# Performance work log

Measured on AMD Instinct MI355X. Metric: run time of the kernel, lower is better.

Reference implementation:

```python
import math
import jax, jax.numpy as jnp
import numpy as np

LOW_FREQ = 1
FACTOR = 1


def setup_inputs() -> dict:
    key = jax.random.key(0)
    x = jax.random.normal(key, (16, 4096, 256), dtype=jnp.float32)
    return {"x": x}


def reference(x):
    b, t, d = x.shape
    x_freq = jnp.fft.rfft(x, axis=1)  # (b, t//2+1, d) complex
    if t % 2 == 0:
        x_freq = x_freq[:, LOW_FREQ:-1]
        f = jnp.fft.rfftfreq(t)[LOW_FREQ:-1]
    else:
        x_freq = x_freq[:, LOW_FREQ:]
        f = jnp.fft.rfftfreq(t)[LOW_FREQ:]
    f = f.astype(jnp.float32)
    F = x_freq.shape[1]
    top_k = int(FACTOR * math.log(F))  # static (shape-derived)

    # top-k by magnitude along freq axis, independently per (b, d)
    xf_bdf = jnp.moveaxis(x_freq, 1, 2)              # (b, d, F)
    _, idx = jax.lax.top_k(jnp.abs(xf_bdf), top_k)   # (b, d, k) int32
    xf_sel = jnp.take_along_axis(xf_bdf, idx, axis=2)  # (b, d, k)
    xf_sel = jnp.moveaxis(xf_sel, 2, 1)              # (b, k, d)
    f_sel = jnp.moveaxis(f[idx], 2, 1)[:, :, None, :]  # (b, k, 1, d)

    # extrapolate: conj-pair frequencies, synthesize cosines, reduce over freq
    xf2 = jnp.concatenate([xf_sel, jnp.conj(xf_sel)], axis=1)  # (b, 2k, d)
    f2 = jnp.concatenate([f_sel, -f_sel], axis=1)              # (b, 2k, 1, d)
    tt = jnp.arange(t, dtype=jnp.float32)[None, None, :, None]  # (1,1,t,1)
    amp = (jnp.abs(xf2) * 2.0 / t)[:, :, None, :]   # (b, 2k, 1, d)
    phase = jnp.angle(xf2)[:, :, None, :]           # (b, 2k, 1, d)
    x_time = amp * jnp.cos(2.0 * math.pi * f2 * tt + phase)  # (b, 2k, t, d)
    return x_time.sum(axis=1)  # (b, t, d)
```

## Files before the change

### kernel.cpp

```cpp
#include <hip/hip_runtime.h>
#include <math.h>

#define T_LEN 4096
#define N2    2048
#define TOPK  7
#define NCH   256
#define R8F 0.70710678f

#define AD(a) ((a) + ((a) >> 3) + ((a) >> 8))

typedef float nt_f4 __attribute__((ext_vector_type(4)));

typedef float2 c32;
__device__ __forceinline__ c32 cadd(c32 a, c32 b) { return make_float2(a.x + b.x, a.y + b.y); }
__device__ __forceinline__ c32 csub(c32 a, c32 b) { return make_float2(a.x - b.x, a.y - b.y); }
__device__ __forceinline__ c32 cmul(c32 a, c32 w) {
    return make_float2(w.x * a.x - w.y * a.y, w.x * a.y + w.y * a.x);
}
__device__ __forceinline__ c32 csq(c32 a) {
    return make_float2(a.x * a.x - a.y * a.y, 2.0f * a.x * a.y);
}
__device__ __forceinline__ c32 mulnegi(c32 a) { return make_float2(a.y, -a.x); }

__device__ __forceinline__ void dft8_pw(c32 x[8], c32 w1)
{
    c32 t0 = cadd(x[0], x[4]), t4 = csub(x[0], x[4]);
    c32 t1 = cadd(x[1], x[5]), t5 = csub(x[1], x[5]);
    c32 t2 = cadd(x[2], x[6]), t6 = csub(x[2], x[6]);
    c32 t3 = cadd(x[3], x[7]), t7 = csub(x[3], x[7]);
    c32 s0 = cadd(t0, t2), s2 = csub(t0, t2);
    c32 s1 = cadd(t1, t3), s3 = csub(t1, t3);
    x[0] = cadd(s0, s1);
    x[4] = csub(s0, s1);
    c32 s3n = mulnegi(s3);
    x[2] = cadd(s2, s3n);
    x[6] = csub(s2, s3n);
    c32 c1 = make_float2(R8F * (t5.x + t5.y), R8F * (t5.y - t5.x));
    c32 c2 = mulnegi(t6);
    c32 c3 = make_float2(R8F * (t7.y - t7.x), -R8F * (t7.x + t7.y));
    c32 d0 = cadd(t4, c2), d1 = csub(t4, c2);
    c32 d2 = cadd(c1, c3), d3 = csub(c1, c3);
    x[1] = cadd(d0, d2);
    x[5] = csub(d0, d2);
    c32 d3n = mulnegi(d3);
    x[3] = cadd(d1, d3n);
    x[7] = csub(d1, d3n);

    c32 w2 = csq(w1);
    c32 w3 = cmul(w1, w2);
    c32 w4 = csq(w2);
    c32 w5 = cmul(w3, w2);
    c32 w6 = csq(w3);
    c32 w7 = cmul(w4, w3);
    x[1] = cmul(x[1], w1);
    x[2] = cmul(x[2], w2);
    x[3] = cmul(x[3], w3);
    x[4] = cmul(x[4], w4);
    x[5] = cmul(x[5], w5);
    x[6] = cmul(x[6], w6);
    x[7] = cmul(x[7], w7);
}

__global__ __launch_bounds__(256) void prep_kernel(
    const float* __restrict__ x, float2* __restrict__ gz,
    double2* __restrict__ tw, float2* __restrict__ twf)
{
    if (blockIdx.x < 16) {
        int p = blockIdx.x * 256 + threadIdx.x;
        double th = -2.0 * 3.14159265358979323846 * (double)p / (double)T_LEN;
        double c = cos(th), s = sin(th);
        tw[p]  = make_double2(c, s);
        twf[p] = make_float2((float)c, (float)s);
        return;
    }
    __shared__ float tile[256][32];
    const int bid = blockIdx.x - 16;
    const int jt = bid & 15;
    const int ct = (bid >> 4) & 7;
    const int b  = bid >> 7;
    const int j0 = jt << 4, c0 = ct << 5;
    const int tid = threadIdx.x;

    const float* src = x + (size_t)b * T_LEN * NCH + c0;
#pragma unroll
    for (int s = 0; s < 8; ++s) {
        int fid = tid + (s << 8);
        int lr  = fid >> 3;
        int qc  = (fid & 7) << 2;
        int t   = (j0 << 1) + ((lr >> 5) << 9) + (lr & 31);
        nt_f4 v = __builtin_nontemporal_load(
            (const nt_f4*)(src + (size_t)t * NCH + qc));
        int sc = qc ^ ((((lr & 7) ^ ((lr >> 3) & 7))) << 2);
        *(nt_f4*)&tile[lr][sc] = v;
    }
    __syncthreads();

    const int dj = tid & 15;
    const int j  = j0 + dj;
    float ang = (float)j * -0.00306796157577128218f;
    float s1v, c1v;
    __sincosf(ang, &s1v, &c1v);
    c32 w1 = make_float2(c1v, s1v);

    for (int h = 0; h < 2; ++h) {
        const int cc = (tid >> 4) + (h << 4);
        c32 xx[8];
#pragma unroll
        for (int u = 0; u < 8; ++u) {
            int lr0 = (u << 5) + (dj << 1);
            int lr1 = lr0 + 1;
            int s0  = cc ^ ((((lr0 & 7) ^ ((lr0 >> 3) & 7))) << 2);
            int s1  = cc ^ ((((lr1 & 7) ^ ((lr1 >> 3) & 7))) << 2);
            xx[u] = make_float2(tile[lr0][s0], tile[lr1][s1]);
        }
        dft8_pw(xx, w1);
        float2* gcol = gz + ((size_t)((b << 8) + c0 + cc)) * N2;
#pragma unroll
        for (int m = 0; m < 8; ++m)
            gcol[(m << 8) + j] = xx[m];
    }
}

__device__ __forceinline__ unsigned long long packkey32(float mag, int k) {
    return ((unsigned long long)__float_as_uint(mag) << 32)
         | (unsigned long long)(2047 - k);
}

#define CSWAP(i, j) { unsigned long long a_ = keys[i], b_ = keys[j]; \
                      keys[i] = a_ > b_ ? a_ : b_; keys[j] = a_ > b_ ? b_ : a_; }

__global__ __launch_bounds__(256, 8) void fft_topk_kernel(
    const float* __restrict__ xt, const double2* __restrict__ tw,
    const float2* __restrict__ twf,
    int* __restrict__ k_out, float4* __restrict__ ab4)
{
    __shared__ float2 zz[AD(N2 - 1) + 3];
    __shared__ unsigned long long wavetop[4 * TOPK];
    __shared__ unsigned long long selkey[TOPK];

    const int tid = threadIdx.x;
    const int bc  = blockIdx.x;
    const float2* gcol = ((const float2*)xt) + (size_t)bc * N2;

    c32 x[8];
    {
        const int g = tid >> 5, j2 = tid & 31, base = (g << 8) + j2;
#pragma unroll
        for (int u = 0; u < 8; ++u)
            x[u] = gcol[base + (u << 5)];
        dft8_pw(x, twf[16 * j2]);
#pragma unroll
        for (int m = 0; m < 8; ++m)
            zz[AD(base + (m << 5))] = x[m];
    }
    __syncthreads();

    {
        const int g3 = tid >> 2, j3 = tid & 3, base = (g3 << 5) + j3;
#pragma unroll
        for (int u = 0; u < 8; ++u)
            x[u] = zz[AD(base + (u << 2))];
        dft8_pw(x, twf[128 * j3]);
#pragma unroll
        for (int m = 0; m < 8; ++m)
            zz[AD(base + (m << 2))] = x[m];
    }
    __syncthreads();

#pragma unroll
    for (int q = 0; q < 2; ++q) {
        int h4 = ((q << 8) + tid) << 2;
#pragma unroll
        for (int r = 0; r < 4; ++r)
            x[q * 4 + r] = zz[AD(h4 + r)];
    }
    __syncthreads();
#pragma unroll
    for (int q = 0; q < 2; ++q) {
        c32 b0 = x[q*4+0], b1 = x[q*4+1], b2 = x[q*4+2], b3 = x[q*4+3];
        c32 e0 = cadd(b0, b2), e1 = csub(b0, b2);
        c32 e2 = cadd(b1, b3), e3 = csub(b1, b3);
        c32 e3n = mulnegi(e3);
        int kbase = ((tid & 7) << 6) | (((tid >> 3) & 7) << 3) | (q << 2) | (tid >> 6);
        zz[AD(kbase)]        = cadd(e0, e2);
        zz[AD(kbase + 1024)] = csub(e0, e2);
        zz[AD(kbase +  512)] = cadd(e1, e3n);
        zz[AD(kbase + 1536)] = csub(e1, e3n);
    }
    __syncthreads();

    unsigned long long keys[8];
#pragma unroll
    for (int j = 0; j < 4; ++j) {
        int k  = 1 + tid + (j << 8);
        int kp = N2 - k;
        float2 yk = zz[AD(k)];
        float2 yp = zz[AD(kp)];
        float Ar = 0.5f * (yk.x + yp.x), Ai = 0.5f * (yk.y - yp.y);
        float Br = 0.5f * (yk.y + yp.y), Bi = -0.5f * (yk.x - yp.x);
        float2 t = twf[k];
        float Cr = t.x * Br - t.y * Bi;
        float Ci = t.x * Bi + t.y * Br;
        float m1 = (Ar + Cr) * (Ar + Cr) + (Ai + Ci) * (Ai + Ci);
        float m2 = (Ar - Cr) * (Ar - Cr) + (Ai - Ci) * (Ai - Ci);
        keys[2 * j]     = packkey32(m1, k);
        keys[2 * j + 1] = (kp != k) ? packkey32(m2, kp) : 0ULL;
    }

    CSWAP(0,1) CSWAP(2,3) CSWAP(4,5) CSWAP(6,7)
    CSWAP(0,2) CSWAP(1,3) CSWAP(4,6) CSWAP(5,7)
    CSWAP(1,2) CSWAP(5,6)
    CSWAP(0,4) CSWAP(1,5) CSWAP(2,6) CSWAP(3,7)
    CSWAP(2,4) CSWAP(3,5)
    CSWAP(1,2) CSWAP(3,4) CSWAP(5,6)

    const int wv = tid >> 6, ln = tid & 63;
    unsigned long long lb = keys[0];

    for (int it = 0; it < TOPK; ++it) {
        unsigned int hl = (unsigned int)(lb >> 32);
        unsigned int h  = hl;
#pragma unroll
        for (int off = 32; off; off >>= 1) {
            unsigned int o = __shfl_xor(h, off);
            h = (o > h) ? o : h;
        }
        unsigned long long mask = __ballot(hl == h);
        unsigned long long v;
        if (__popcll(mask) == 1) {
            int src = __ffsll((long long)mask) - 1;
            v = ((unsigned long long)h << 32)
              | (unsigned long long)__shfl((unsigned int)lb, src);
        } else {
            unsigned int l = (hl == h) ? (unsigned int)lb : 0u;
#pragma unroll
            for (int off = 32; off; off >>= 1) {
                unsigned int o = __shfl_xor(l, off);
                l = (o > l) ? o : l;
            }
            v = ((unsigned long long)h << 32) | l;
        }
        if (ln == 0) wavetop[wv * TOPK + it] = v;
        if (v == lb && v) {
            keys[0]=keys[1]; keys[1]=keys[2]; keys[2]=keys[3]; keys[3]=keys[4];
            keys[4]=keys[5]; keys[5]=keys[6]; keys[6]=keys[7]; keys[7]=0ULL;
            lb = keys[0];
        }
    }
    __syncthreads();

    if (tid < 32) {
        unsigned long long v = (tid < 4 * TOPK) ? wavetop[tid] : 0ULL;
        for (int it = 0; it < TOPK; ++it) {
            unsigned long long m = v;
#pragma unroll
            for (int off = 16; off; off >>= 1) {
                unsigned long long o = __shfl_xor(m, off);
                if (o > m) m = o;
            }
            if (tid == 0) selkey[it] = m;
            if (m == v) v = 0ULL;
        }
    }
    __syncthreads();

    if (tid < TOPK) {
        int k  = 2047 - (int)(selkey[tid] & 2047ULL);
        float2 ykf = zz[AD(k)];
        float2 ypf = zz[AD(N2 - k)];
        double ykx = (double)ykf.x, yky = (double)ykf.y;
        double ypx = (double)ypf.x, ypy = (double)ypf.y;
        double Ar = 0.5 * (ykx + ypx), Ai = 0.5 * (yky - ypy);
        double Br = 0.5 * (yky + ypy), Bi = -0.5 * (ykx - ypx);
        double2 t = tw[k];
        double Xr = Ar + t.x * Br - t.y * Bi;
        double Xi = Ai + t.x * Bi + t.y * Br;
        k_out[tid * 4096 + bc] = k;
        ab4[tid * 4096 + bc] = make_float4(
            (float)( 4.0 * Xr / (double)T_LEN),
            (float)(-4.0 * Xi / (double)T_LEN),
            (float)t.x, (float)(-t.y));
    }
}

__global__ __launch_bounds__(256) void recon_kernel(
    const int* __restrict__ k_in, const float4* __restrict__ ab4,
    float* __restrict__ out)
{
    __shared__ float tile[16][256];

    const int tid   = threadIdx.x;
    const int chunk = blockIdx.x & 127;
    const int b     = blockIdx.x >> 7;
    const int bc    = (b << 8) + tid;
    const int n0    = chunk << 5;

    const float c0 = 6.28318530717958647692f / 4096.0f;
    float aa[TOPK], bb[TOPK];
    c32 z[TOPK], w[TOPK];
#pragma unroll
    for (int j = 0; j < TOPK; ++j) {
        int k    = k_in[j * 4096 + bc];
        float4 v = ab4[j * 4096 + bc];
        aa[j] = v.x; bb[j] = v.y; w[j] = make_float2(v.z, v.w);
        int m0 = (k * n0) & (T_LEN - 1);
        float ang = (float)m0 * c0;
        __sincosf(ang, &z[j].y, &z[j].x);
    }

    float* obase = out + ((size_t)b * T_LEN + n0) * NCH;
    for (int r = 0; r < 2; ++r) {
#pragma unroll
        for (int i = 0; i < 16; ++i) {
            float acc = 0.f;
#pragma unroll
            for (int j = 0; j < TOPK; ++j) {
                acc += aa[j] * z[j].x + bb[j] * z[j].y;
                z[j] = cmul(z[j], w[j]);
            }
            tile[i][tid] = acc;
        }
        __syncthreads();
#pragma unroll
        for (int s = 0; s < 4; ++s) {
            int fid = tid + (s << 8);
            int ni  = fid >> 6;
            int c4  = (fid & 63) << 2;
            nt_f4 v = { tile[ni][c4], tile[ni][c4 + 1],
                        tile[ni][c4 + 2], tile[ni][c4 + 3] };
            __builtin_nontemporal_store(v,
                (nt_f4*)(obase + (size_t)((r << 4) + ni) * NCH + c4));
        }
        __syncthreads();
    }
}

extern "C" void kernel_launch(void* const* d_in, const int* in_sizes, int n_in,
                              void* d_out, int out_size, void* d_ws, size_t ws_size,
                              hipStream_t stream) {
    const float* x   = (const float*)d_in[0];
    float*       out = (float*)d_out;
    char*        ws  = (char*)d_ws;

    double2* tw    = (double2*)(ws);
    int*     k_ws  = (int*)   (ws + 65536);
    float4*  ab_ws = (float4*)(ws + 180224);
    float2*  twf   = (float2*)(ws + 638976);

    prep_kernel     <<<16 + 2048, 256, 0, stream>>>(x, (float2*)out, tw, twf);
    fft_topk_kernel <<<4096, 256, 0, stream>>>(out, tw, twf, k_ws, ab_ws);
    recon_kernel    <<<2048, 256, 0, stream>>>(k_ws, ab_ws, out);
}
```

Before: 170.2 us.

## Process two channels per block in FFT top-k kernel

```diff
diff --git a/kernel.cpp b/kernel.cpp
--- a/kernel.cpp
+++ b/kernel.cpp
@@ -22,7 +22,7 @@
 }
 __device__ __forceinline__ c32 mulnegi(c32 a) { return make_float2(a.y, -a.x); }
 
-__device__ __forceinline__ void dft8_pw(c32 x[8], c32 w1)
+__device__ __forceinline__ void dft8_core(c32 x[8])
 {
     c32 t0 = cadd(x[0], x[4]), t4 = csub(x[0], x[4]);
     c32 t1 = cadd(x[1], x[5]), t5 = csub(x[1], x[5]);
@@ -45,7 +45,11 @@
     c32 d3n = mulnegi(d3);
     x[3] = cadd(d1, d3n);
     x[7] = csub(d1, d3n);
-
+}
+
+__device__ __forceinline__ void dft8_pw(c32 x[8], c32 w1)
+{
+    dft8_core(x);
     c32 w2 = csq(w1);
     c32 w3 = cmul(w1, w2);
     c32 w4 = csq(w2);
@@ -61,6 +65,25 @@
     x[7] = cmul(x[7], w7);
 }
 
+__device__ __forceinline__ void dft8_pw2(c32 xa[8], c32 xb[8], c32 w1)
+{
+    dft8_core(xa);
+    dft8_core(xb);
+    c32 w2 = csq(w1);
+    c32 w3 = cmul(w1, w2);
+    c32 w4 = csq(w2);
+    c32 w5 = cmul(w3, w2);
+    c32 w6 = csq(w3);
+    c32 w7 = cmul(w4, w3);
+    xa[1] = cmul(xa[1], w1); xb[1] = cmul(xb[1], w1);
+    xa[2] = cmul(xa[2], w2); xb[2] = cmul(xb[2], w2);
+    xa[3] = cmul(xa[3], w3); xb[3] = cmul(xb[3], w3);
+    xa[4] = cmul(xa[4], w4); xb[4] = cmul(xb[4], w4);
+    xa[5] = cmul(xa[5], w5); xb[5] = cmul(xb[5], w5);
+    xa[6] = cmul(xa[6], w6); xb[6] = cmul(xb[6], w6);
+    xa[7] = cmul(xa[7], w7); xb[7] = cmul(xb[7], w7);
+}
+
 __global__ __launch_bounds__(256) void prep_kernel(
     const float* __restrict__ x, float2* __restrict__ gz,
     double2* __restrict__ tw, float2* __restrict__ twf)
@@ -126,44 +149,95 @@
          | (unsigned long long)(2047 - k);
 }
 
-#define CSWAP(i, j) { unsigned long long a_ = keys[i], b_ = keys[j]; \
-                      keys[i] = a_ > b_ ? a_ : b_; keys[j] = a_ > b_ ? b_ : a_; }
-
-__global__ __launch_bounds__(256, 8) void fft_topk_kernel(
+#define CSWAP(K, i, j) { unsigned long long a_ = K[i], b_ = K[j]; \
+                         K[i] = a_ > b_ ? a_ : b_; K[j] = a_ > b_ ? b_ : a_; }
+#define SORT8(K) \
+    CSWAP(K,0,1) CSWAP(K,2,3) CSWAP(K,4,5) CSWAP(K,6,7) \
+    CSWAP(K,0,2) CSWAP(K,1,3) CSWAP(K,4,6) CSWAP(K,5,7) \
+    CSWAP(K,1,2) CSWAP(K,5,6) \
+    CSWAP(K,0,4) CSWAP(K,1,5) CSWAP(K,2,6) CSWAP(K,3,7) \
+    CSWAP(K,2,4) CSWAP(K,3,5) \
+    CSWAP(K,1,2) CSWAP(K,3,4) CSWAP(K,5,6)
+
+__device__ __forceinline__ void sel_round(
+    unsigned long long keys[8], unsigned long long& lb,
+    unsigned long long* wavetop, int wv, int ln, int it)
+{
+    unsigned int hl = (unsigned int)(lb >> 32);
+    unsigned int h  = hl;
+#pragma unroll
+    for (int off = 32; off; off >>= 1) {
+        unsigned int o = __shfl_xor(h, off);
+        h = (o > h) ? o : h;
+    }
+    unsigned long long mask = __ballot(hl == h);
+    unsigned long long v;
+    if (__popcll(mask) == 1) {
+        int src = __ffsll((long long)mask) - 1;
+        v = ((unsigned long long)h << 32)
+          | (unsigned long long)__shfl((unsigned int)lb, src);
+    } else {
+        unsigned int l = (hl == h) ? (unsigned int)lb : 0u;
+#pragma unroll
+        for (int off = 32; off; off >>= 1) {
+            unsigned int o = __shfl_xor(l, off);
+            l = (o > l) ? o : l;
+        }
+        v = ((unsigned long long)h << 32) | l;
+    }
+    if (ln == 0) wavetop[wv * TOPK + it] = v;
+    if (v == lb && v) {
+        keys[0]=keys[1]; keys[1]=keys[2]; keys[2]=keys[3]; keys[3]=keys[4];
+        keys[4]=keys[5]; keys[5]=keys[6]; keys[6]=keys[7]; keys[7]=0ULL;
+        lb = keys[0];
+    }
+}
+
+__global__ __launch_bounds__(256, 4) void fft_topk_kernel(
     const float* __restrict__ xt, const double2* __restrict__ tw,
     const float2* __restrict__ twf,
     int* __restrict__ k_out, float4* __restrict__ ab4)
 {
-    __shared__ float2 zz[AD(N2 - 1) + 3];
-    __shared__ unsigned long long wavetop[4 * TOPK];
-    __shared__ unsigned long long selkey[TOPK];
+    __shared__ float2 zzA[AD(N2 - 1) + 3];
+    __shared__ float2 zzB[AD(N2 - 1) + 3];
+    __shared__ unsigned long long wavetopA[4 * TOPK], wavetopB[4 * TOPK];
+    __shared__ unsigned long long selkeyA[TOPK], selkeyB[TOPK];
 
     const int tid = threadIdx.x;
-    const int bc  = blockIdx.x;
-    const float2* gcol = ((const float2*)xt) + (size_t)bc * N2;
-
-    c32 x[8];
+    const int bcA = blockIdx.x * 2;
+    const float2* gA = ((const float2*)xt) + (size_t)bcA * N2;
+    const float2* gB = gA + N2;
+
+    c32 xa[8], xb[8];
     {
         const int g = tid >> 5, j2 = tid & 31, base = (g << 8) + j2;
 #pragma unroll
-        for (int u = 0; u < 8; ++u)
-            x[u] = gcol[base + (u << 5)];
-        dft8_pw(x, twf[16 * j2]);
-#pragma unroll
-        for (int m = 0; m < 8; ++m)
-            zz[AD(base + (m << 5))] = x[m];
+        for (int u = 0; u < 8; ++u) {
+            xa[u] = gA[base + (u << 5)];
+            xb[u] = gB[base + (u << 5)];
+        }
+        dft8_pw2(xa, xb, twf[16 * j2]);
+#pragma unroll
+        for (int m = 0; m < 8; ++m) {
+            int ad = AD(base + (m << 5));
+            zzA[ad] = xa[m]; zzB[ad] = xb[m];
+        }
     }
     __syncthreads();
 
     {
         const int g3 = tid >> 2, j3 = tid & 3, base = (g3 << 5) + j3;
 #pragma unroll
-        for (int u = 0; u < 8; ++u)
-            x[u] = zz[AD(base + (u << 2))];
-        dft8_pw(x, twf[128 * j3]);
-#pragma unroll
-        for (int m = 0; m < 8; ++m)
-            zz[AD(base + (m << 2))] = x[m];
+        for (int u = 0; u < 8; ++u) {
+            int ad = AD(base + (u << 2));
+            xa[u] = zzA[ad]; xb[u] = zzB[ad];
+        }
+        dft8_pw2(xa, xb, twf[128 * j3]);
+#pragma unroll
+        for (int m = 0; m < 8; ++m) {
+            int ad = AD(base + (m << 2));
+            zzA[ad] = xa[m]; zzB[ad] = xb[m];
+        }
     }
     __syncthreads();
 
@@ -171,86 +245,87 @@
     for (int q = 0; q < 2; ++q) {
         int h4 = ((q << 8) + tid) << 2;
 #pragma unroll
-        for (int r = 0; r < 4; ++r)
-            x[q * 4 + r] = zz[AD(h4 + r)];
+        for (int r = 0; r < 4; ++r) {
+            int ad = AD(h4 + r);
+            xa[q * 4 + r] = zzA[ad]; xb[q * 4 + r] = zzB[ad];
+        }
     }
     __syncthreads();
 #pragma unroll
     for (int q = 0; q < 2; ++q) {
-        c32 b0 = x[q*4+0], b1 = x[q*4+1], b2 = x[q*4+2], b3 = x[q*4+3];
-        c32 e0 = cadd(b0, b2), e1 = csub(b0, b2);
-        c32 e2 = cadd(b1, b3), e3 = csub(b1, b3);
-        c32 e3n = mulnegi(e3);
         int kbase = ((tid & 7) << 6) | (((tid >> 3) & 7) << 3) | (q << 2) | (tid >> 6);
-        zz[AD(kbase)]        = cadd(e0, e2);
-        zz[AD(kbase + 1024)] = csub(e0, e2);
-        zz[AD(kbase +  512)] = cadd(e1, e3n);
-        zz[AD(kbase + 1536)] = csub(e1, e3n);
-    }
-    __syncthreads();
-
-    unsigned long long keys[8];
+        {
+            c32 b0 = xa[q*4+0], b1 = xa[q*4+1], b2 = xa[q*4+2], b3 = xa[q*4+3];
+            c32 e0 = cadd(b0, b2), e1 = csub(b0, b2);
+            c32 e2 = cadd(b1, b3), e3 = csub(b1, b3);
+            c32 e3n = mulnegi(e3);
+            zzA[AD(kbase)]        = cadd(e0, e2);
+            zzA[AD(kbase + 1024)] = csub(e0, e2);
+            zzA[AD(kbase +  512)] = cadd(e1, e3n);
+            zzA[AD(kbase + 1536)] = csub(e1, e3n);
+        }
+        {
+            c32 b0 = xb[q*4+0], b1 = xb[q*4+1], b2 = xb[q*4+2], b3 = xb[q*4+3];
+            c32 e0 = cadd(b0, b2), e1 = csub(b0, b2);
+            c32 e2 = cadd(b1, b3), e3 = csub(b1, b3);
+            c32 e3n = mulnegi(e3);
+            zzB[AD(kbase)]        = cadd(e0, e2);
+            zzB[AD(kbase + 1024)] = csub(e0, e2);
+            zzB[AD(kbase +  512)] = cadd(e1, e3n);
+            zzB[AD(kbase + 1536)] = csub(e1, e3n);
+        }
+    }
+    __syncthreads();
+
+    unsigned long long keysA[8], keysB[8];
 #pragma unroll
     for (int j = 0; j < 4; ++j) {
         int k  = 1 + tid + (j << 8);
         int kp = N2 - k;
-        float2 yk = zz[AD(k)];
-        float2 yp = zz[AD(kp)];
-        float Ar = 0.5f * (yk.x + yp.x), Ai = 0.5f * (yk.y - yp.y);
-        float Br = 0.5f * (yk.y + yp.y), Bi = -0.5f * (yk.x - yp.x);
+        int adk = AD(k), adp = AD(kp);
         float2 t = twf[k];
-        float Cr = t.x * Br - t.y * Bi;
-        float Ci = t.x * Bi + t.y * Br;
-        float m1 = (Ar + Cr) * (Ar + Cr) + (Ai + Ci) * (Ai + Ci);
-        float m2 = (Ar - Cr) * (Ar - Cr) + (Ai - Ci) * (Ai - Ci);
-        keys[2 * j]     = packkey32(m1, k);
-        keys[2 * j + 1] = (kp != k) ? packkey32(m2, kp) : 0ULL;
-    }
-
-    CSWAP(0,1) CSWAP(2,3) CSWAP(4,5) CSWAP(6,7)
-    CSWAP(0,2) CSWAP(1,3) CSWAP(4,6) CSWAP(5,7)
-    CSWAP(1,2) CSWAP(5,6)
-    CSWAP(0,4) CSWAP(1,5) CSWAP(2,6) CSWAP(3,7)
-    CSWAP(2,4) CSWAP(3,5)
-    CSWAP(1,2) CSWAP(3,4) CSWAP(5,6)
+        {
+            float2 yk = zzA[adk], yp = zzA[adp];
+            float Ar = 0.5f * (yk.x + yp.x), Ai = 0.5f * (yk.y - yp.y);
+            float Br = 0.5f * (yk.y + yp.y), Bi = -0.5f * (yk.x - yp.x);
+            float Cr = t.x * Br - t.y * Bi;
+            float Ci = t.x * Bi + t.y * Br;
+            float m1 = (Ar + Cr) * (Ar + Cr) + (Ai + Ci) * (Ai + Ci);
+            float m2 = (Ar - Cr) * (Ar - Cr) + (Ai - Ci) * (Ai - Ci);
+            keysA[2 * j]     = packkey32(m1, k);
+            keysA[2 * j + 1] = (kp != k) ? packkey32(m2, kp) : 0ULL;
+        }
+        {
+            float2 yk = zzB[adk], yp = zzB[adp];
+            float Ar = 0.5f * (yk.x + yp.x), Ai = 0.5f * (yk.y - yp.y);
+            float Br = 0.5f * (yk.y + yp.y), Bi = -0.5f * (yk.x - yp.x);
+            float Cr = t.x * Br - t.y * Bi;
+            float Ci = t.x * Bi + t.y * Br;
+            float m1 = (Ar + Cr) * (Ar + Cr) + (Ai + Ci) * (Ai + Ci);
+            float m2 = (Ar - Cr) * (Ar - Cr) + (Ai - Ci) * (Ai - Ci);
+            keysB[2 * j]     = packkey32(m1, k);
+            keysB[2 * j + 1] = (kp != k) ? packkey32(m2, kp) : 0ULL;
+        }
+    }
+
+    SORT8(keysA)
+    SORT8(keysB)
 
     const int wv = tid >> 6, ln = tid & 63;
-    unsigned long long lb = keys[0];
+    unsigned long long lbA = keysA[0], lbB = keysB[0];
 
     for (int it = 0; it < TOPK; ++it) {
-        unsigned int hl = (unsigned int)(lb >> 32);
-        unsigned int h  = hl;
-#pragma unroll
-        for (int off = 32; off; off >>= 1) {
-            unsigned int o = __shfl_xor(h, off);
-            h = (o > h) ? o : h;
-        }
-        unsigned long long mask = __ballot(hl == h);
-        unsigned long long v;
-        if (__popcll(mask) == 1) {
-            int src = __ffsll((long long)mask) - 1;
-            v = ((unsigned long long)h << 32)
-              | (unsigned long long)__shfl((unsigned int)lb, src);
-        } else {
-            unsigned int l = (hl == h) ? (unsigned int)lb : 0u;
-#pragma unroll
-            for (int off = 32; off; off >>= 1) {
-                unsigned int o = __shfl_xor(l, off);
-                l = (o > l) ? o : l;
-            }
-            v = ((unsigned long long)h << 32) | l;
-        }
-        if (ln == 0) wavetop[wv * TOPK + it] = v;
-        if (v == lb && v) {
-            keys[0]=keys[1]; keys[1]=keys[2]; keys[2]=keys[3]; keys[3]=keys[4];
-            keys[4]=keys[5]; keys[5]=keys[6]; keys[6]=keys[7]; keys[7]=0ULL;
-            lb = keys[0];
-        }
-    }
-    __syncthreads();
-
-    if (tid < 32) {
-        unsigned long long v = (tid < 4 * TOPK) ? wavetop[tid] : 0ULL;
+        sel_round(keysA, lbA, wavetopA, wv, ln, it);
+        sel_round(keysB, lbB, wavetopB, wv, ln, it);
+    }
+    __syncthreads();
+
+    if (tid < 64) {
+        const bool isB = tid >= 32;
+        const int  sl  = tid & 31;
+        const unsigned long long* wt = isB ? wavetopB : wavetopA;
+        unsigned long long* sk = isB ? selkeyB : selkeyA;
+        unsigned long long v = (sl < 4 * TOPK) ? wt[sl] : 0ULL;
         for (int it = 0; it < TOPK; ++it) {
             unsigned long long m = v;
 #pragma unroll
@@ -258,14 +333,18 @@
                 unsigned long long o = __shfl_xor(m, off);
                 if (o > m) m = o;
             }
-            if (tid == 0) selkey[it] = m;
+            if (sl == 0) sk[it] = m;
             if (m == v) v = 0ULL;
         }
     }
     __syncthreads();
 
-    if (tid < TOPK) {
-        int k  = 2047 - (int)(selkey[tid] & 2047ULL);
+    if (tid < TOPK || (tid >= 64 && tid < 64 + TOPK)) {
+        const bool isB = tid >= 64;
+        const int  sl  = isB ? tid - 64 : tid;
+        const int  bc  = bcA + (isB ? 1 : 0);
+        const float2* zz = isB ? zzB : zzA;
+        int k  = 2047 - (int)((isB ? selkeyB[sl] : selkeyA[sl]) & 2047ULL);
         float2 ykf = zz[AD(k)];
         float2 ypf = zz[AD(N2 - k)];
         double ykx = (double)ykf.x, yky = (double)ykf.y;
@@ -275,8 +354,8 @@
         double2 t = tw[k];
         double Xr = Ar + t.x * Br - t.y * Bi;
         double Xi = Ai + t.x * Bi + t.y * Br;
-        k_out[tid * 4096 + bc] = k;
-        ab4[tid * 4096 + bc] = make_float4(
+        k_out[sl * 4096 + bc] = k;
+        ab4[sl * 4096 + bc] = make_float4(
             (float)( 4.0 * Xr / (double)T_LEN),
             (float)(-4.0 * Xi / (double)T_LEN),
             (float)t.x, (float)(-t.y));
@@ -348,6 +427,6 @@
     float2*  twf   = (float2*)(ws + 638976);
 
     prep_kernel     <<<16 + 2048, 256, 0, stream>>>(x, (float2*)out, tw, twf);
-    fft_topk_kernel <<<4096, 256, 0, stream>>>(out, tw, twf, k_ws, ab_ws);
+    fft_topk_kernel <<<2048, 256, 0, stream>>>(out, tw, twf, k_ws, ab_ws);
     recon_kernel    <<<2048, 256, 0, stream>>>(k_ws, ab_ws, out);
 }
```

Measured after the change: 168.4 us. About the same (-1.1%).
